# Performance work log

Measured on AMD Instinct MI355X. Metric: run time of the kernel, lower is better.

Reference implementation:

```python
import jax, jax.numpy as jnp
import numpy as np

B, U, L, H, M = 4, 16, 128, 768, 256   # docs, utterances/doc, tokens/utt, hidden, mentions/doc
HID = 150                               # Score MLP hidden dim
N_CLUSTERS = 32


def setup_inputs() -> dict:
    key = jax.random.key(0)
    ks = jax.random.split(key, 8)
    hidden = jax.random.normal(ks[0], (B, U, L, H), jnp.float32)

    rng = np.random.default_rng(0)
    span_utt = rng.integers(0, U, (B, M))
    span_start = rng.integers(0, L - 8, (B, M))
    span_end = span_start + rng.integers(1, 9, (B, M))  # span length in [1, 8]

    # coreference labels: label[i, j] = 1 iff j is a true antecedent (j < i, same cluster);
    # if mention i has no antecedent, label[i, i] = 1 (the epsilon / new-entity slot).
    clusters = rng.integers(0, N_CLUSTERS, (B, M))
    same = clusters[:, :, None] == clusters[:, None, :]
    ant = same & np.tril(np.ones((M, M), bool), -1)
    labels = ant.astype(np.float32)
    diag = np.arange(M)
    labels[:, diag, diag] = (~ant.any(-1)).astype(np.float32)

    scale = 0.02
    W1 = jax.random.normal(ks[1], (3 * H, HID), jnp.float32) * scale
    W2 = jax.random.normal(ks[2], (HID, HID), jnp.float32) * scale
    W3 = jax.random.normal(ks[3], (HID, 1), jnp.float32) * scale
    return {
        "hidden": hidden,
        "span_utt": jnp.asarray(span_utt, jnp.int32),
        "span_start": jnp.asarray(span_start, jnp.int32),
        "span_end": jnp.asarray(span_end, jnp.int32),
        "labels": jnp.asarray(labels),
        "W1": W1, "b1": jnp.zeros((HID,), jnp.float32),
        "W2": W2, "b2": jnp.zeros((HID,), jnp.float32),
        "W3": W3, "b3": jnp.zeros((1,), jnp.float32),
    }


def reference(hidden, span_utt, span_start, span_end, labels, W1, b1, W2, b2, W3, b3):
    # ---- span mean-pooling (EntityEncoder, aggr='mean') ----
    pos = jnp.arange(L)
    mask = (pos[None, None, :] >= span_start[..., None]) & (pos[None, None, :] < span_end[..., None])
    w = mask.astype(hidden.dtype) / (span_end - span_start)[..., None].astype(hidden.dtype)  # [B,M,L]
    gathered = jnp.take_along_axis(hidden, span_utt[:, :, None, None], axis=1)  # [B,M,L,H]
    pooled = jnp.einsum('bml,bmlh->bmh', w, gathered)  # [B,M,H]

    # ---- pairwise antecedent scoring (PairScorer / Score MLP, dropout=eval) ----
    ii, jj = np.tril_indices(M, -1)  # static pair indices, P = M(M-1)/2
    # concat(i_g, j_g, i_g*j_g) @ W1  ==  i_g@W1a + j_g@W1b + (i_g*j_g)@W1c
    W1a, W1b, W1c = W1[:H], W1[H:2 * H], W1[2 * H:]
    hi = pooled @ W1a   # [B,M,HID]
    hj = pooled @ W1b   # [B,M,HID]
    prod = pooled[:, ii] * pooled[:, jj]                    # [B,P,H]
    h1 = jax.nn.relu(hi[:, ii] + hj[:, jj] + prod @ W1c + b1)
    h2 = jax.nn.relu(h1 @ W2 + b2)
    s = (h2 @ W3 + b3)[..., 0]  # [B,P]

    # ---- per-mention ragged softmax, padded to [M, M] with -1000 ----
    # row i has logits s_ij for j<i plus epsilon=0 at j=i (diagonal of zeros matrix)
    logits = jnp.zeros((B, M, M), hidden.dtype).at[:, ii, jj].set(s)
    valid = jnp.tril(jnp.ones((M, M), bool))
    probs = jax.nn.softmax(jnp.where(valid, logits, -1e30), axis=-1)
    probs = jnp.where(valid, probs, jnp.asarray(-1000.0, hidden.dtype))

    # ---- compute_loss ----
    eps = 1e-8
    prob_sum = jnp.sum(jnp.clip(probs * labels, eps, 1.0 - eps), axis=-1)  # [B,M]
    loss = -jnp.sum(jnp.log(prob_sum))
    return loss
```

## Files before the change

### kernel.cpp

```cpp
#include <hip/hip_runtime.h>
#include <hip/hip_bf16.h>

#define B_ 4
#define U_ 16
#define L_ 128
#define H_ 768
#define M_ 256
#define HID_ 150

typedef _Float16 half8 __attribute__((ext_vector_type(8)));
typedef _Float16 half4t __attribute__((ext_vector_type(4)));
typedef float floatx4 __attribute__((ext_vector_type(4)));
typedef float floatx16 __attribute__((ext_vector_type(16)));

#define MFMA32(wf, af, acc) __builtin_amdgcn_mfma_f32_32x32x16_f16(wf, af, acc, 0, 0, 0)

__global__ __launch_bounds__(256) void prep_pool_kernel(
    const float* __restrict__ W1, const float* __restrict__ W2,
    const float* __restrict__ b2, const float* __restrict__ W3,
    const float* __restrict__ hidden, const int* __restrict__ sutt,
    const int* __restrict__ sstart, const int* __restrict__ send,
    _Float16* __restrict__ W1cs, _Float16* __restrict__ W2s,
    _Float16* __restrict__ W1abs, float2* __restrict__ bw,
    _Float16* __restrict__ pooledh)
{
    if (blockIdx.x >= 1540) {
        const int bm = (blockIdx.x - 1540) * 4 + (threadIdx.x >> 6);
        const int lane = threadIdx.x & 63;
        const int b  = bm >> 8;
        const int u  = sutt[bm];
        const int st = sstart[bm];
        const int en = send[bm];
        const float inv = 1.0f / (float)(en - st);
        const float* src = hidden + ((size_t)(b * U_ + u) * L_) * H_ + lane * 12;
        float4 s[3];
        #pragma unroll
        for (int q = 0; q < 3; ++q) s[q] = make_float4(0.f, 0.f, 0.f, 0.f);
        for (int l = st; l < en; ++l) {
            const float* p = src + (size_t)l * H_;
            #pragma unroll
            for (int q = 0; q < 3; ++q) {
                float4 v = *(const float4*)(p + q * 4);
                s[q].x += v.x; s[q].y += v.y; s[q].z += v.z; s[q].w += v.w;
            }
        }
        _Float16* gp = pooledh + (size_t)bm * H_ + lane * 12;
        #pragma unroll
        for (int q = 0; q < 3; ++q) {
            half4t hv;
            hv[0] = (_Float16)(s[q].x * inv); hv[1] = (_Float16)(s[q].y * inv);
            hv[2] = (_Float16)(s[q].z * inv); hv[3] = (_Float16)(s[q].w * inv);
            *(half4t*)(gp + q * 4) = hv;
        }
        return;
    }
    int idx = blockIdx.x * 256 + threadIdx.x;
    if (blockIdx.x == 0 && threadIdx.x < 160) {
        int n = threadIdx.x;
        bw[n] = (n < HID_) ? make_float2(b2[n], W3[n]) : make_float2(0.f, 0.f);
    }
    if (idx < 122880) {
        int k = idx / 160, n = idx - k * 160;
        float v = (n < HID_) ? W1[(size_t)(2 * H_ + k) * HID_ + n] : 0.f;
        W1cs[(k >> 4) * 2560 + (n >> 5) * 512 +
             (((n & 31) | (((k >> 3) & 1) << 5)) << 3) + (k & 7)] = (_Float16)v;
        return;
    }
    idx -= 122880;
    if (idx < 25600) {
        int k = idx / 160, n = idx - k * 160;
        float v = (k < HID_ && n < HID_) ? W2[(size_t)k * HID_ + n] : 0.f;
        W2s[(k >> 4) * 2560 + (n >> 5) * 512 +
            (((n & 31) | (((k >> 3) & 1) << 5)) << 3) + (k & 7)] = (_Float16)v;
        return;
    }
    idx -= 25600;
    if (idx < 245760) {
        int k = idx / 320, n = idx - k * 320;
        float v = 0.f;
        if (n < HID_) v = W1[(size_t)k * HID_ + n];
        else if (n >= 160 && n < 160 + HID_) v = W1[(size_t)(H_ + k) * HID_ + (n - 160)];
        W1abs[(k >> 5) * 10240 + (n >> 4) * 512 +
              (((n & 15) | (((k >> 3) & 3) << 4)) << 3) + (k & 7)] = (_Float16)v;
    }
}

__global__ __launch_bounds__(256) void hihj_kernel(
    const _Float16* __restrict__ pooledh, const float* __restrict__ b1,
    const _Float16* __restrict__ W1abs,
    float* __restrict__ hiF, float* __restrict__ hjT, float* __restrict__ out)
{
    if (blockIdx.x == 0 && threadIdx.x == 0) *out = 0.f;
    __shared__ __align__(16) _Float16 spool[16 * 776];
    const int blk = blockIdx.x;
    const int tid = threadIdx.x;
    for (int e = tid; e < 16 * 96; e += 256) {
        int r = e / 96, c = e - r * 96;
        *(half8*)&spool[r * 776 + c * 8] =
            *(const half8*)&pooledh[(size_t)(blk * 16 + r) * H_ + c * 8];
    }
    __syncthreads();

    const int w = tid >> 6, lane = tid & 63;
    const int g = lane >> 4, l15 = lane & 15;
    floatx4 acc[5];
    #pragma unroll
    for (int u5 = 0; u5 < 5; ++u5) acc[u5] = (floatx4){0.f, 0.f, 0.f, 0.f};
    const _Float16* aB = &spool[l15 * 776 + g * 8];
    for (int kc = 0; kc < 24; ++kc) {
        half8 av = *(const half8*)(aB + kc * 32);
        #pragma unroll
        for (int u5 = 0; u5 < 5; ++u5) {
            const int u = w * 5 + u5;
            half8 bv = *(const half8*)(W1abs + (size_t)((kc * 20 + u) * 64 + lane) * 8);
            acc[u5] = __builtin_amdgcn_mfma_f32_16x16x32_f16(av, bv, acc[u5], 0, 0, 0);
        }
    }
    const int row0 = blk * 16 + g * 4;
    #pragma unroll
    for (int u5 = 0; u5 < 5; ++u5) {
        const int n = (w * 5 + u5) * 16 + l15;
        if (n < HID_) {
            float b1v = b1[n];
            #pragma unroll
            for (int r = 0; r < 4; ++r)
                hiF[(size_t)(row0 + r) * 160 + n] = acc[u5][r] + b1v;
        } else if (n >= 160 && n < 160 + HID_) {
            *(float4*)&hjT[(size_t)(n - 160) * 1024 + row0] =
                make_float4(acc[u5][0], acc[u5][1], acc[u5][2], acc[u5][3]);
        }
    }
}

__global__ __launch_bounds__(256, 1) void pair_mlp_kernel(
    const _Float16* __restrict__ pooledh,
    const float* __restrict__ hiF, const float* __restrict__ hjT,
    const _Float16* __restrict__ W1cs, const _Float16* __restrict__ W2s,
    const float2* __restrict__ bw, const float* __restrict__ b3,
    float* __restrict__ logits)
{
    __shared__ __align__(16) _Float16 sW[2][10240];
    __shared__ __align__(16) _Float16 h1L[4][64 * 170];

    const int b = blockIdx.y;
    int t = blockIdx.x;
    int jt = 0;
    while (t >= 32 - 4 * jt) { t -= 32 - 4 * jt; ++jt; }
    const int tid = threadIdx.x;
    const int w = tid >> 6, lane = tid & 63;
    const int p = 16 * jt + 4 * t + w;
    const int i0 = 2 * p, j0 = 32 * jt;
    const int bm = b * M_;
    const int c31 = lane & 31, hw = lane >> 5;

    const _Float16* pjp  = pooledh + (size_t)(bm + j0 + c31) * H_ + (hw << 3);
    const _Float16* pip0 = pooledh + (size_t)(bm + i0) * H_ + (hw << 3);
    const _Float16* pip1 = pooledh + (size_t)(bm + i0 + 1) * H_ + (hw << 3);

    floatx16 acc1[2][5];
    #pragma unroll
    for (int tt = 0; tt < 2; ++tt)
        #pragma unroll
        for (int t1 = 0; t1 < 5; ++t1)
            #pragma unroll
            for (int e = 0; e < 16; ++e) acc1[tt][t1][e] = 0.f;

    half8 Apj[2][4], Ai0[2][4], Ai1[2][4], stg[2][5];

    #pragma unroll
    for (int q = 0; q < 5; ++q)
        stg[0][q] = *(const half8*)(W1cs + (size_t)(tid + q * 256) * 8);
    #pragma unroll
    for (int h = 0; h < 4; ++h) {
        Apj[0][h] = *(const half8*)(pjp + h * 16);
        Ai0[0][h] = *(const half8*)(pip0 + h * 16);
        Ai1[0][h] = *(const half8*)(pip1 + h * 16);
    }
    #pragma unroll
    for (int q = 0; q < 5; ++q)
        *(half8*)&sW[0][(tid + q * 256) * 8] = stg[0][q];
    __syncthreads();

    #pragma unroll
    for (int sc = 0; sc < 12; ++sc) {
        const int cur = sc & 1, nxt = cur ^ 1;
        if (sc < 11) {
            const _Float16* wg = W1cs + (size_t)(sc + 1) * 10240;
            #pragma unroll
            for (int q = 0; q < 5; ++q)
                stg[nxt][q] = *(const half8*)(wg + (size_t)(tid + q * 256) * 8);
            const int kb = (sc + 1) * 64;
            #pragma unroll
            for (int h = 0; h < 4; ++h) {
                Apj[nxt][h] = *(const half8*)(pjp + kb + h * 16);
                Ai0[nxt][h] = *(const half8*)(pip0 + kb + h * 16);
                Ai1[nxt][h] = *(const half8*)(pip1 + kb + h * 16);
            }
        }
        #pragma unroll
        for (int h = 0; h < 4; ++h) {
            half8 a0 = Ai0[cur][h] * Apj[cur][h];
            half8 a1 = Ai1[cur][h] * Apj[cur][h];
            #pragma unroll
            for (int t1 = 0; t1 < 5; ++t1) {
                half8 wf = *(const half8*)&sW[cur][h * 2560 + t1 * 512 + lane * 8];
                acc1[0][t1] = MFMA32(wf, a0, acc1[0][t1]);
                acc1[1][t1] = MFMA32(wf, a1, acc1[1][t1]);
            }
        }
        if (sc < 11) {
            #pragma unroll
            for (int q = 0; q < 5; ++q)
                *(half8*)&sW[nxt][(tid + q * 256) * 8] = stg[nxt][q];
            __syncthreads();
        }
    }

    _Float16* h1w = h1L[w];
    #pragma unroll
    for (int t1 = 0; t1 < 5; ++t1) {
        #pragma unroll
        for (int qd = 0; qd < 4; ++qd) {
            const int n1 = t1 * 32 + 8 * qd + 4 * hw;
            float hj0 = hjT[(size_t)(n1 + 0) * 1024 + bm + j0 + c31];
            float hj1 = hjT[(size_t)(n1 + 1) * 1024 + bm + j0 + c31];
            float hj2 = hjT[(size_t)(n1 + 2) * 1024 + bm + j0 + c31];
            float hj3 = hjT[(size_t)(n1 + 3) * 1024 + bm + j0 + c31];
            #pragma unroll
            for (int tt = 0; tt < 2; ++tt) {
                float4 hiv = *(const float4*)&hiF[(size_t)(bm + i0 + tt) * 160 + n1];
                half4t hv;
                hv[0] = (_Float16)fmaxf(acc1[tt][t1][4 * qd + 0] + hiv.x + hj0, 0.f);
                hv[1] = (_Float16)fmaxf(acc1[tt][t1][4 * qd + 1] + hiv.y + hj1, 0.f);
                hv[2] = (_Float16)fmaxf(acc1[tt][t1][4 * qd + 2] + hiv.z + hj2, 0.f);
                hv[3] = (_Float16)fmaxf(acc1[tt][t1][4 * qd + 3] + hiv.w + hj3, 0.f);
                *(half4t*)&h1w[(tt * 32 + c31) * 170 + n1] = hv;
            }
        }
    }

    floatx16 acc2[2][5];
    #pragma unroll
    for (int tt = 0; tt < 2; ++tt)
        #pragma unroll
        for (int t2 = 0; t2 < 5; ++t2)
            #pragma unroll
            for (int e = 0; e < 16; ++e) acc2[tt][t2][e] = 0.f;

    half8 W2f[3][5];
    #pragma unroll
    for (int c = 0; c < 3; ++c) {
        const _Float16* wb = W2s + (size_t)(c * 5) * 512 + lane * 8;
        #pragma unroll
        for (int t2 = 0; t2 < 5; ++t2) W2f[c][t2] = *(const half8*)(wb + t2 * 512);
    }
    #pragma unroll
    for (int kc2 = 0; kc2 < 10; ++kc2) {
        const int cur = kc2 % 3;
        half8 h0 = *(const half8*)&h1w[c31 * 170 + kc2 * 16 + hw * 8];
        half8 h1f = *(const half8*)&h1w[(32 + c31) * 170 + kc2 * 16 + hw * 8];
        #pragma unroll
        for (int t2 = 0; t2 < 5; ++t2) {
            acc2[0][t2] = MFMA32(W2f[cur][t2], h0, acc2[0][t2]);
            acc2[1][t2] = MFMA32(W2f[cur][t2], h1f, acc2[1][t2]);
        }
        if (kc2 < 7) {
            const _Float16* wb = W2s + (size_t)((kc2 + 3) * 5) * 512 + lane * 8;
            #pragma unroll
            for (int t2 = 0; t2 < 5; ++t2)
                W2f[cur][t2] = *(const half8*)(wb + t2 * 512);
        }
    }

    const float b3v = b3[0];
    #pragma unroll
    for (int tt = 0; tt < 2; ++tt) {
        float sown = 0.f;
        #pragma unroll
        for (int t2 = 0; t2 < 5; ++t2) {
            #pragma unroll
            for (int qd = 0; qd < 4; ++qd) {
                const int n2 = t2 * 32 + 8 * qd + 4 * hw;
                float4 bw01 = *(const float4*)&bw[n2];
                float4 bw23 = *(const float4*)&bw[n2 + 2];
                sown += fmaxf(acc2[tt][t2][4 * qd + 0] + bw01.x, 0.f) * bw01.y;
                sown += fmaxf(acc2[tt][t2][4 * qd + 1] + bw01.z, 0.f) * bw01.w;
                sown += fmaxf(acc2[tt][t2][4 * qd + 2] + bw23.x, 0.f) * bw23.y;
                sown += fmaxf(acc2[tt][t2][4 * qd + 3] + bw23.z, 0.f) * bw23.w;
            }
        }
        float s = sown + __shfl_xor(sown, 32);
        const int i = i0 + tt;
        const int j = j0 + c31;
        if (lane < 32 && j < i)
            logits[(size_t)(bm + i) * M_ + j] = s + b3v;
    }
}

__global__ __launch_bounds__(256) void loss_kernel(
    const float* __restrict__ logits, const float* __restrict__ labels,
    float* __restrict__ out)
{
    const int bm = blockIdx.x;
    const int i  = bm & (M_ - 1);
    const int j  = threadIdx.x;
    __shared__ float red[4];
    __shared__ float bcast;

    float val = (j < i) ? logits[(size_t)bm * M_ + j]
                        : ((j == i) ? 0.0f : -1e30f);

    float m = val;
    #pragma unroll
    for (int off = 32; off >= 1; off >>= 1) m = fmaxf(m, __shfl_down(m, off, 64));
    const int wave = j >> 6, lane = j & 63;
    if (lane == 0) red[wave] = m;
    __syncthreads();
    if (j == 0) bcast = fmaxf(fmaxf(red[0], red[1]), fmaxf(red[2], red[3]));
    __syncthreads();
    const float mm = bcast;

    float e = (j <= i) ? expf(val - mm) : 0.0f;
    float s = e;
    #pragma unroll
    for (int off = 32; off >= 1; off >>= 1) s += __shfl_down(s, off, 64);
    __syncthreads();
    if (lane == 0) red[wave] = s;
    __syncthreads();
    if (j == 0) bcast = red[0] + red[1] + red[2] + red[3];
    __syncthreads();
    const float ssum = bcast;

    float prob = (j <= i) ? (e / ssum) : -1000.0f;
    float lab = labels[(size_t)bm * M_ + j];
    float tv = prob * lab;
    tv = fminf(fmaxf(tv, 1e-8f), 1.0f - 1e-8f);
    float rs = tv;
    #pragma unroll
    for (int off = 32; off >= 1; off >>= 1) rs += __shfl_down(rs, off, 64);
    __syncthreads();
    if (lane == 0) red[wave] = rs;
    __syncthreads();
    if (j == 0) atomicAdd(out, -logf(red[0] + red[1] + red[2] + red[3]));
}

extern "C" void kernel_launch(void* const* d_in, const int* in_sizes, int n_in,
                              void* d_out, int out_size, void* d_ws, size_t ws_size,
                              hipStream_t stream)
{
    const float* hidden = (const float*)d_in[0];
    const int*   sutt   = (const int*)d_in[1];
    const int*   sstart = (const int*)d_in[2];
    const int*   send   = (const int*)d_in[3];
    const float* labels = (const float*)d_in[4];
    const float* W1     = (const float*)d_in[5];
    const float* b1     = (const float*)d_in[6];
    const float* W2     = (const float*)d_in[7];
    const float* b2     = (const float*)d_in[8];
    const float* W3     = (const float*)d_in[9];
    const float* b3     = (const float*)d_in[10];

    float* ws = (float*)d_ws;
    float*    hiF     = ws;
    float*    hjT     = ws + 163840;
    float*    logits  = ws + 327680;
    float2*   bw      = (float2*)(ws + 589824);
    _Float16* pooledh = (_Float16*)(ws + 590144);
    _Float16* W1cs    = (_Float16*)(ws + 983360);
    _Float16* W2s     = (_Float16*)(ws + 1106240);
    _Float16* W1abs   = (_Float16*)(ws + 1119040);
    float* out = (float*)d_out;

    prep_pool_kernel<<<dim3(1796), 256, 0, stream>>>(
        W1, W2, b2, W3, hidden, sutt, sstart, send,
        W1cs, W2s, W1abs, bw, pooledh);
    hihj_kernel<<<dim3(64), 256, 0, stream>>>(pooledh, b1, W1abs, hiF, hjT, out);
    pair_mlp_kernel<<<dim3(144, B_), 256, 0, stream>>>(pooledh, hiF, hjT,
                                                       W1cs, W2s, bw, b3, logits);
    loss_kernel<<<dim3(B_ * M_), 256, 0, stream>>>(logits, labels, out);
}
```

Measured before the change: 228.4 us.

## Use single-wave blocks with 4-row i tiles for pair MLP and hihj

The pair MLP kernel moves from 4-wave blocks that share W1c through double-buffered LDS to 1-wave blocks. Each block handles 4 i-rows by 32 j-columns, staging only pooled_j in LDS and reading W1c fragments straight from global/L2. Layer 2 now runs in two halves to keep register pressure down. hihj is also split into 64-thread blocks over a 2D grid with no LDS staging. The aim is more blocks, finer triangular scheduling and no block barriers, at the cost of more global weight traffic per block and high register use.

```diff
diff --git a/kernel.cpp b/kernel.cpp
--- a/kernel.cpp
+++ b/kernel.cpp
@@ -14,6 +14,8 @@
 typedef float floatx16 __attribute__((ext_vector_type(16)));
 
 #define MFMA32(wf, af, acc) __builtin_amdgcn_mfma_f32_32x32x16_f16(wf, af, acc, 0, 0, 0)
+
+union H8 { half8 v; half4t h[2]; };
 
 __global__ __launch_bounds__(256) void prep_pool_kernel(
     const float* __restrict__ W1, const float* __restrict__ W2,
@@ -85,41 +87,33 @@
     }
 }
 
-__global__ __launch_bounds__(256) void hihj_kernel(
+__global__ __launch_bounds__(64) void hihj_kernel(
     const _Float16* __restrict__ pooledh, const float* __restrict__ b1,
     const _Float16* __restrict__ W1abs,
     float* __restrict__ hiF, float* __restrict__ hjT, float* __restrict__ out)
 {
-    if (blockIdx.x == 0 && threadIdx.x == 0) *out = 0.f;
-    __shared__ __align__(16) _Float16 spool[16 * 776];
-    const int blk = blockIdx.x;
-    const int tid = threadIdx.x;
-    for (int e = tid; e < 16 * 96; e += 256) {
-        int r = e / 96, c = e - r * 96;
-        *(half8*)&spool[r * 776 + c * 8] =
-            *(const half8*)&pooledh[(size_t)(blk * 16 + r) * H_ + c * 8];
-    }
-    __syncthreads();
-
-    const int w = tid >> 6, lane = tid & 63;
+    if (blockIdx.x == 0 && blockIdx.y == 0 && threadIdx.x == 0) *out = 0.f;
+    const int rowblk = blockIdx.x;
+    const int nq     = blockIdx.y;
+    const int lane = threadIdx.x & 63;
     const int g = lane >> 4, l15 = lane & 15;
     floatx4 acc[5];
     #pragma unroll
     for (int u5 = 0; u5 < 5; ++u5) acc[u5] = (floatx4){0.f, 0.f, 0.f, 0.f};
-    const _Float16* aB = &spool[l15 * 776 + g * 8];
+    const _Float16* aB = pooledh + (size_t)(rowblk * 16 + l15) * H_ + g * 8;
     for (int kc = 0; kc < 24; ++kc) {
         half8 av = *(const half8*)(aB + kc * 32);
         #pragma unroll
         for (int u5 = 0; u5 < 5; ++u5) {
-            const int u = w * 5 + u5;
+            const int u = nq * 5 + u5;
             half8 bv = *(const half8*)(W1abs + (size_t)((kc * 20 + u) * 64 + lane) * 8);
             acc[u5] = __builtin_amdgcn_mfma_f32_16x16x32_f16(av, bv, acc[u5], 0, 0, 0);
         }
     }
-    const int row0 = blk * 16 + g * 4;
+    const int row0 = rowblk * 16 + g * 4;
     #pragma unroll
     for (int u5 = 0; u5 < 5; ++u5) {
-        const int n = (w * 5 + u5) * 16 + l15;
+        const int n = (nq * 5 + u5) * 16 + l15;
         if (n < HID_) {
             float b1v = b1[n];
             #pragma unroll
@@ -132,168 +126,170 @@
     }
 }
 
-__global__ __launch_bounds__(256, 1) void pair_mlp_kernel(
+__global__ __launch_bounds__(64, 1) void pair_mlp_kernel(
     const _Float16* __restrict__ pooledh,
     const float* __restrict__ hiF, const float* __restrict__ hjT,
     const _Float16* __restrict__ W1cs, const _Float16* __restrict__ W2s,
     const float2* __restrict__ bw, const float* __restrict__ b3,
     float* __restrict__ logits)
 {
-    __shared__ __align__(16) _Float16 sW[2][10240];
-    __shared__ __align__(16) _Float16 h1L[4][64 * 170];
-
-    const int b = blockIdx.y;
-    int t = blockIdx.x;
-    int jt = 0;
-    while (t >= 32 - 4 * jt) { t -= 32 - 4 * jt; ++jt; }
-    const int tid = threadIdx.x;
-    const int w = tid >> 6, lane = tid & 63;
-    const int p = 16 * jt + 4 * t + w;
-    const int i0 = 2 * p, j0 = 32 * jt;
+    __shared__ __align__(16) _Float16 pjL[2 * 32 * 68];
+    __shared__ __align__(16) _Float16 h1L[2 * 32 * 164];
+
+    int q = blockIdx.x;
+    const int b = q / 288;
+    int r = q - b * 288;
+    int h = 0;
+    while (r >= 8 * (h + 1)) { r -= 8 * (h + 1); ++h; }
+    const int g = 8 * h + r / (h + 1);
+    const int jt = r - (r / (h + 1)) * (h + 1);
+    const int i0 = 4 * g, j0 = 32 * jt;
     const int bm = b * M_;
+    const int lane = threadIdx.x & 63;
     const int c31 = lane & 31, hw = lane >> 5;
 
-    const _Float16* pjp  = pooledh + (size_t)(bm + j0 + c31) * H_ + (hw << 3);
-    const _Float16* pip0 = pooledh + (size_t)(bm + i0) * H_ + (hw << 3);
-    const _Float16* pip1 = pooledh + (size_t)(bm + i0 + 1) * H_ + (hw << 3);
-
-    floatx16 acc1[2][5];
-    #pragma unroll
-    for (int tt = 0; tt < 2; ++tt)
+    floatx16 acc1[4][5];
+    #pragma unroll
+    for (int tt = 0; tt < 4; ++tt)
         #pragma unroll
         for (int t1 = 0; t1 < 5; ++t1)
             #pragma unroll
             for (int e = 0; e < 16; ++e) acc1[tt][t1][e] = 0.f;
 
-    half8 Apj[2][4], Ai0[2][4], Ai1[2][4], stg[2][5];
-
-    #pragma unroll
-    for (int q = 0; q < 5; ++q)
-        stg[0][q] = *(const half8*)(W1cs + (size_t)(tid + q * 256) * 8);
-    #pragma unroll
-    for (int h = 0; h < 4; ++h) {
-        Apj[0][h] = *(const half8*)(pjp + h * 16);
-        Ai0[0][h] = *(const half8*)(pip0 + h * 16);
-        Ai1[0][h] = *(const half8*)(pip1 + h * 16);
-    }
-    #pragma unroll
-    for (int q = 0; q < 5; ++q)
-        *(half8*)&sW[0][(tid + q * 256) * 8] = stg[0][q];
-    __syncthreads();
-
-    #pragma unroll
-    for (int sc = 0; sc < 12; ++sc) {
-        const int cur = sc & 1, nxt = cur ^ 1;
-        if (sc < 11) {
-            const _Float16* wg = W1cs + (size_t)(sc + 1) * 10240;
-            #pragma unroll
-            for (int q = 0; q < 5; ++q)
-                stg[nxt][q] = *(const half8*)(wg + (size_t)(tid + q * 256) * 8);
-            const int kb = (sc + 1) * 64;
-            #pragma unroll
-            for (int h = 0; h < 4; ++h) {
-                Apj[nxt][h] = *(const half8*)(pjp + kb + h * 16);
-                Ai0[nxt][h] = *(const half8*)(pip0 + kb + h * 16);
-                Ai1[nxt][h] = *(const half8*)(pip1 + kb + h * 16);
-            }
-        }
-        #pragma unroll
-        for (int h = 0; h < 4; ++h) {
-            half8 a0 = Ai0[cur][h] * Apj[cur][h];
-            half8 a1 = Ai1[cur][h] * Apj[cur][h];
+    const int srow = j0 + (lane >> 3);
+    const int sseg = (lane & 7) * 8;
+    const _Float16* pjg = pooledh + (size_t)(bm + srow) * H_ + sseg;
+
+    {
+        half8 sj[4];
+        #pragma unroll
+        for (int q2 = 0; q2 < 4; ++q2)
+            sj[q2] = *(const half8*)(pjg + (size_t)(q2 * 8) * H_);
+        #pragma unroll
+        for (int q2 = 0; q2 < 4; ++q2) {
+            H8 u2; u2.v = sj[q2];
+            _Float16* d = &pjL[((q2 * 8 + (lane >> 3))) * 68 + sseg];
+            *(half4t*)d = u2.h[0];
+            *(half4t*)(d + 4) = u2.h[1];
+        }
+    }
+
+    #pragma unroll 2
+    for (int c = 0; c < 12; ++c) {
+        const int cur = c & 1;
+        half8 sj[4];
+        if (c < 11) {
+            const int kb = (c + 1) * 64;
+            #pragma unroll
+            for (int q2 = 0; q2 < 4; ++q2)
+                sj[q2] = *(const half8*)(pjg + (size_t)(q2 * 8) * H_ + kb);
+        }
+        #pragma unroll
+        for (int ks = 0; ks < 4; ++ks) {
+            H8 pj;
+            const _Float16* rb = &pjL[cur * 2176 + c31 * 68 + ks * 16 + hw * 8];
+            pj.h[0] = *(const half4t*)rb;
+            pj.h[1] = *(const half4t*)(rb + 4);
+            half8 prod[4];
+            #pragma unroll
+            for (int tt = 0; tt < 4; ++tt) {
+                half8 pif = *(const half8*)(pooledh +
+                    (size_t)(bm + i0 + tt) * H_ + c * 64 + ks * 16 + hw * 8);
+                prod[tt] = pif * pj.v;
+            }
+            const _Float16* wb = W1cs + (size_t)(c * 4 + ks) * 2560 + lane * 8;
             #pragma unroll
             for (int t1 = 0; t1 < 5; ++t1) {
-                half8 wf = *(const half8*)&sW[cur][h * 2560 + t1 * 512 + lane * 8];
-                acc1[0][t1] = MFMA32(wf, a0, acc1[0][t1]);
-                acc1[1][t1] = MFMA32(wf, a1, acc1[1][t1]);
-            }
-        }
-        if (sc < 11) {
-            #pragma unroll
-            for (int q = 0; q < 5; ++q)
-                *(half8*)&sW[nxt][(tid + q * 256) * 8] = stg[nxt][q];
-            __syncthreads();
-        }
-    }
-
-    _Float16* h1w = h1L[w];
-    #pragma unroll
-    for (int t1 = 0; t1 < 5; ++t1) {
-        #pragma unroll
-        for (int qd = 0; qd < 4; ++qd) {
-            const int n1 = t1 * 32 + 8 * qd + 4 * hw;
-            float hj0 = hjT[(size_t)(n1 + 0) * 1024 + bm + j0 + c31];
-            float hj1 = hjT[(size_t)(n1 + 1) * 1024 + bm + j0 + c31];
-            float hj2 = hjT[(size_t)(n1 + 2) * 1024 + bm + j0 + c31];
-            float hj3 = hjT[(size_t)(n1 + 3) * 1024 + bm + j0 + c31];
-            #pragma unroll
-            for (int tt = 0; tt < 2; ++tt) {
-                float4 hiv = *(const float4*)&hiF[(size_t)(bm + i0 + tt) * 160 + n1];
-                half4t hv;
-                hv[0] = (_Float16)fmaxf(acc1[tt][t1][4 * qd + 0] + hiv.x + hj0, 0.f);
-                hv[1] = (_Float16)fmaxf(acc1[tt][t1][4 * qd + 1] + hiv.y + hj1, 0.f);
-                hv[2] = (_Float16)fmaxf(acc1[tt][t1][4 * qd + 2] + hiv.z + hj2, 0.f);
-                hv[3] = (_Float16)fmaxf(acc1[tt][t1][4 * qd + 3] + hiv.w + hj3, 0.f);
-                *(half4t*)&h1w[(tt * 32 + c31) * 170 + n1] = hv;
-            }
-        }
-    }
-
-    floatx16 acc2[2][5];
-    #pragma unroll
-    for (int tt = 0; tt < 2; ++tt)
-        #pragma unroll
-        for (int t2 = 0; t2 < 5; ++t2)
-            #pragma unroll
-            for (int e = 0; e < 16; ++e) acc2[tt][t2][e] = 0.f;
-
-    half8 W2f[3][5];
-    #pragma unroll
-    for (int c = 0; c < 3; ++c) {
-        const _Float16* wb = W2s + (size_t)(c * 5) * 512 + lane * 8;
-        #pragma unroll
-        for (int t2 = 0; t2 < 5; ++t2) W2f[c][t2] = *(const half8*)(wb + t2 * 512);
-    }
-    #pragma unroll
-    for (int kc2 = 0; kc2 < 10; ++kc2) {
-        const int cur = kc2 % 3;
-        half8 h0 = *(const half8*)&h1w[c31 * 170 + kc2 * 16 + hw * 8];
-        half8 h1f = *(const half8*)&h1w[(32 + c31) * 170 + kc2 * 16 + hw * 8];
-        #pragma unroll
-        for (int t2 = 0; t2 < 5; ++t2) {
-            acc2[0][t2] = MFMA32(W2f[cur][t2], h0, acc2[0][t2]);
-            acc2[1][t2] = MFMA32(W2f[cur][t2], h1f, acc2[1][t2]);
-        }
-        if (kc2 < 7) {
-            const _Float16* wb = W2s + (size_t)((kc2 + 3) * 5) * 512 + lane * 8;
+                half8 wf = *(const half8*)(wb + t1 * 512);
+                acc1[0][t1] = MFMA32(wf, prod[0], acc1[0][t1]);
+                acc1[1][t1] = MFMA32(wf, prod[1], acc1[1][t1]);
+                acc1[2][t1] = MFMA32(wf, prod[2], acc1[2][t1]);
+                acc1[3][t1] = MFMA32(wf, prod[3], acc1[3][t1]);
+            }
+        }
+        if (c < 11) {
+            _Float16* dbase = &pjL[(cur ^ 1) * 2176];
+            #pragma unroll
+            for (int q2 = 0; q2 < 4; ++q2) {
+                H8 u2; u2.v = sj[q2];
+                _Float16* d = dbase + (q2 * 8 + (lane >> 3)) * 68 + sseg;
+                *(half4t*)d = u2.h[0];
+                *(half4t*)(d + 4) = u2.h[1];
+            }
+        }
+    }
+
+    const float b3v = b3[0];
+    #pragma unroll
+    for (int tp = 0; tp < 2; ++tp) {
+        #pragma unroll
+        for (int t1 = 0; t1 < 5; ++t1) {
+            #pragma unroll
+            for (int qd = 0; qd < 4; ++qd) {
+                const int n1 = t1 * 32 + 8 * qd + 4 * hw;
+                float hj0 = hjT[(size_t)(n1 + 0) * 1024 + bm + j0 + c31];
+                float hj1 = hjT[(size_t)(n1 + 1) * 1024 + bm + j0 + c31];
+                float hj2 = hjT[(size_t)(n1 + 2) * 1024 + bm + j0 + c31];
+                float hj3 = hjT[(size_t)(n1 + 3) * 1024 + bm + j0 + c31];
+                #pragma unroll
+                for (int lt = 0; lt < 2; ++lt) {
+                    const int tt = 2 * tp + lt;
+                    float4 hiv = *(const float4*)&hiF[(size_t)(bm + i0 + tt) * 160 + n1];
+                    half4t hv;
+                    hv[0] = (_Float16)fmaxf(acc1[tt][t1][4 * qd + 0] + hiv.x + hj0, 0.f);
+                    hv[1] = (_Float16)fmaxf(acc1[tt][t1][4 * qd + 1] + hiv.y + hj1, 0.f);
+                    hv[2] = (_Float16)fmaxf(acc1[tt][t1][4 * qd + 2] + hiv.z + hj2, 0.f);
+                    hv[3] = (_Float16)fmaxf(acc1[tt][t1][4 * qd + 3] + hiv.w + hj3, 0.f);
+                    *(half4t*)&h1L[lt * 5248 + c31 * 164 + n1] = hv;
+                }
+            }
+        }
+        floatx16 acc2[2][5];
+        #pragma unroll
+        for (int lt = 0; lt < 2; ++lt)
             #pragma unroll
             for (int t2 = 0; t2 < 5; ++t2)
-                W2f[cur][t2] = *(const half8*)(wb + t2 * 512);
-        }
-    }
-
-    const float b3v = b3[0];
-    #pragma unroll
-    for (int tt = 0; tt < 2; ++tt) {
-        float sown = 0.f;
-        #pragma unroll
-        for (int t2 = 0; t2 < 5; ++t2) {
-            #pragma unroll
-            for (int qd = 0; qd < 4; ++qd) {
-                const int n2 = t2 * 32 + 8 * qd + 4 * hw;
-                float4 bw01 = *(const float4*)&bw[n2];
-                float4 bw23 = *(const float4*)&bw[n2 + 2];
-                sown += fmaxf(acc2[tt][t2][4 * qd + 0] + bw01.x, 0.f) * bw01.y;
-                sown += fmaxf(acc2[tt][t2][4 * qd + 1] + bw01.z, 0.f) * bw01.w;
-                sown += fmaxf(acc2[tt][t2][4 * qd + 2] + bw23.x, 0.f) * bw23.y;
-                sown += fmaxf(acc2[tt][t2][4 * qd + 3] + bw23.z, 0.f) * bw23.w;
-            }
-        }
-        float s = sown + __shfl_xor(sown, 32);
-        const int i = i0 + tt;
-        const int j = j0 + c31;
-        if (lane < 32 && j < i)
-            logits[(size_t)(bm + i) * M_ + j] = s + b3v;
+                #pragma unroll
+                for (int e = 0; e < 16; ++e) acc2[lt][t2][e] = 0.f;
+        #pragma unroll
+        for (int kc2 = 0; kc2 < 10; ++kc2) {
+            H8 hf[2];
+            #pragma unroll
+            for (int lt = 0; lt < 2; ++lt) {
+                const _Float16* hb = &h1L[lt * 5248 + c31 * 164 + kc2 * 16 + hw * 8];
+                hf[lt].h[0] = *(const half4t*)hb;
+                hf[lt].h[1] = *(const half4t*)(hb + 4);
+            }
+            const _Float16* wb = W2s + (size_t)kc2 * 2560 + lane * 8;
+            #pragma unroll
+            for (int t2 = 0; t2 < 5; ++t2) {
+                half8 wf = *(const half8*)(wb + t2 * 512);
+                acc2[0][t2] = MFMA32(wf, hf[0].v, acc2[0][t2]);
+                acc2[1][t2] = MFMA32(wf, hf[1].v, acc2[1][t2]);
+            }
+        }
+        #pragma unroll
+        for (int lt = 0; lt < 2; ++lt) {
+            float sown = 0.f;
+            #pragma unroll
+            for (int t2 = 0; t2 < 5; ++t2) {
+                #pragma unroll
+                for (int qd = 0; qd < 4; ++qd) {
+                    const int n2 = t2 * 32 + 8 * qd + 4 * hw;
+                    float4 bw01 = *(const float4*)&bw[n2];
+                    float4 bw23 = *(const float4*)&bw[n2 + 2];
+                    sown += fmaxf(acc2[lt][t2][4 * qd + 0] + bw01.x, 0.f) * bw01.y;
+                    sown += fmaxf(acc2[lt][t2][4 * qd + 1] + bw01.z, 0.f) * bw01.w;
+                    sown += fmaxf(acc2[lt][t2][4 * qd + 2] + bw23.x, 0.f) * bw23.y;
+                    sown += fmaxf(acc2[lt][t2][4 * qd + 3] + bw23.z, 0.f) * bw23.w;
+                }
+            }
+            float s = sown + __shfl_xor(sown, 32);
+            const int i = i0 + 2 * tp + lt;
+            const int j = j0 + c31;
+            if (lane < 32 && j < i)
+                logits[(size_t)(bm + i) * M_ + j] = s + b3v;
+        }
     }
 }
 
@@ -374,8 +370,8 @@
     prep_pool_kernel<<<dim3(1796), 256, 0, stream>>>(
         W1, W2, b2, W3, hidden, sutt, sstart, send,
         W1cs, W2s, W1abs, bw, pooledh);
-    hihj_kernel<<<dim3(64), 256, 0, stream>>>(pooledh, b1, W1abs, hiF, hjT, out);
-    pair_mlp_kernel<<<dim3(144, B_), 256, 0, stream>>>(pooledh, hiF, hjT,
-                                                       W1cs, W2s, bw, b3, logits);
+    hihj_kernel<<<dim3(64, 4), 64, 0, stream>>>(pooledh, b1, W1abs, hiF, hjT, out);
+    pair_mlp_kernel<<<dim3(1152), 64, 0, stream>>>(pooledh, hiF, hjT,
+                                                   W1cs, W2s, bw, b3, logits);
     loss_kernel<<<dim3(B_ * M_), 256, 0, stream>>>(logits, labels, out);
 }
```

New measurement: 524.1 us. 129% more time.
